# Kernel optimization log

Measured on AMD Instinct MI355X. Metric: run time of the kernel, lower is better.

Reference implementation:

```python
import jax, jax.numpy as jnp
import numpy as np

N = 100_000   # num nodes
E = 1_000_000 # num edges
F = 64        # feat_dim
H = 64        # hidden_dim
D = 64        # embed_dim


def _xavier(key, shape):
    limit = float(np.sqrt(6.0 / (shape[0] + shape[1])))
    return jax.random.uniform(key, shape, jnp.float32, -limit, limit)


def setup_inputs() -> dict:
    key = jax.random.key(0)
    ks = jax.random.split(key, 8)
    x = jax.random.normal(ks[0], (N, F), jnp.float32)
    edge_index = jax.random.randint(ks[1], (2, E), 0, N, dtype=jnp.int64)
    # GCNConv weights stored [in, out] (torch Linear transposed); biases zero-init
    return {
        "x": x,
        "edge_index": edge_index,
        "W1": _xavier(ks[2], (F, H)), "b1": jnp.zeros((H,), jnp.float32),
        "W2": _xavier(ks[3], (H, H)), "b2": jnp.zeros((H,), jnp.float32),
        "W3": _xavier(ks[4], (H, D)), "b3": jnp.zeros((D,), jnp.float32),
        "fw1": _xavier(ks[5], (D, H)), "fb1": jnp.zeros((H,), jnp.float32),
        "fw2": _xavier(ks[6], (H, D)), "fb2": jnp.zeros((D,), jnp.float32),
    }


def _gcn_conv(x, src, dst, dinv, W, b):
    # GCNConv: out = D^{-1/2} (A+I) D^{-1/2} (x W) + b
    h = x @ W                                   # [N, out]
    norm = dinv[src] * dinv[dst]                # [E]
    msg = h[src] * norm[:, None]                # gather + scale: [E, out]
    agg = jax.ops.segment_sum(msg, dst, num_segments=N)
    agg = agg + h * (dinv * dinv)[:, None]      # self-loop term
    return agg + b


def reference(x, edge_index, W1, b1, W2, b2, W3, b3, fw1, fb1, fw2, fb2):
    src, dst = edge_index[0], edge_index[1]
    # degree with self-loops (symmetric normalization)
    deg = jax.ops.segment_sum(jnp.ones((E,), x.dtype), dst, num_segments=N) + 1.0
    dinv = jax.lax.rsqrt(deg)
    # eval mode: dropout(p=0.5, training=False) is identity
    h = jax.nn.relu(_gcn_conv(x, src, dst, dinv, W1, b1))
    h = jax.nn.relu(_gcn_conv(h, src, dst, dinv, W2, b2))
    h = jax.nn.relu(_gcn_conv(h, src, dst, dinv, W3, b3))
    h = jax.nn.relu(h @ fw1 + fb1)
    return h @ fw2 + fb2                        # node embeddings [N, D]
```

## Files before the change

kernel.cpp:

```cpp
#include <hip/hip_runtime.h>
#include <cstdint>
#include <cstddef>


#define CDIV(a, b) (((a) + (b) - 1) / (b))

typedef __attribute__((ext_vector_type(8))) short bf16x8;
typedef __attribute__((ext_vector_type(4))) float f32x4;

static constexpr int BKT_SHIFT = 9;
static constexpr int BKT_NODES = 1 << BKT_SHIFT;
static constexpr int BKT_CAP = 7424;

__device__ __forceinline__ void split_bf(float a, short& hi, short& lo) {
  unsigned u = __float_as_uint(a);
  unsigned r = u + (0x7FFF + ((u >> 16) & 1));
  hi = (short)(r >> 16);
  float hirec = __uint_as_float(r & 0xFFFF0000u);
  float res = a - hirec;
  lo = (short)(__float_as_uint(res) >> 16);
}

__device__ __forceinline__ unsigned short f2bf_rne(float a) {
  unsigned u = __float_as_uint(a);
  u += 0x7FFF + ((u >> 16) & 1);
  return (unsigned short)(u >> 16);
}

__device__ __forceinline__ float4 bf4_to_f4(uint2 u) {
  float4 v;
  v.x = __uint_as_float(u.x << 16);
  v.y = __uint_as_float(u.x & 0xFFFF0000u);
  v.z = __uint_as_float(u.y << 16);
  v.w = __uint_as_float(u.y & 0xFFFF0000u);
  return v;
}

__device__ __forceinline__ void split8(float4 x, float4 y, bf16x8& h, bf16x8& l) {
  float av[8] = {x.x, x.y, x.z, x.w, y.x, y.y, y.z, y.w};
#pragma unroll
  for (int j = 0; j < 8; ++j) {
    short hi, lo;
    split_bf(av[j], hi, lo);
    h[j] = hi;
    l[j] = lo;
  }
}

__device__ __forceinline__ float4 nt_ld4(const float* p) {
  f32x4 v = __builtin_nontemporal_load(reinterpret_cast<const f32x4*>(p));
  float4 r;
  r.x = v[0]; r.y = v[1]; r.z = v[2]; r.w = v[3];
  return r;
}

__global__ __launch_bounds__(256)
void k_bucket(const int* __restrict__ ei, int* __restrict__ bcnt,
              int2* __restrict__ pairs, int E) {
  __shared__ int hist[256], rbase[256], roff[256];
  int t = threadIdx.x;
  int chunk = (E + gridDim.x - 1) / gridDim.x;
  int e0 = blockIdx.x * chunk;
  int e1 = min(e0 + chunk, E);
  hist[t] = 0;
  __syncthreads();
  for (int e = e0 + t; e < e1; e += 256) {
    int d = __builtin_nontemporal_load(&ei[E + e]);
    atomicAdd(&hist[d >> BKT_SHIFT], 1);
  }
  __syncthreads();
  roff[t] = 0;
  rbase[t] = hist[t] ? atomicAdd(&bcnt[t], hist[t]) : 0;
  __syncthreads();
  for (int e = e0 + t; e < e1; e += 256) {
    int d = __builtin_nontemporal_load(&ei[E + e]);
    int s = __builtin_nontemporal_load(&ei[e]);
    int b = d >> BKT_SHIFT;
    int r = atomicAdd(&roff[b], 1);
    int idx = rbase[b] + r;
    if (idx < BKT_CAP) pairs[(size_t)b * BKT_CAP + idx] = make_int2(s, d);
  }
}

__global__ __launch_bounds__(1024)
void k_build(const int2* __restrict__ pairs, const int* __restrict__ bcnt,
             int* __restrict__ row_ptr, float* __restrict__ dinv,
             int* __restrict__ srcs, int N, int E, int K) {
  __shared__ int cnt[BKT_NODES];
  __shared__ int deg[BKT_NODES];
  __shared__ int ebase_sh;
  int b = blockIdx.x;
  int t = threadIdx.x;
  int lo = b << BKT_SHIFT;
  int range = min(BKT_NODES, N - lo);
  int sz = min(bcnt[b], BKT_CAP);
  if (t == 0) {
    int s = 0;
    for (int i = 0; i < b; ++i) s += bcnt[i];
    ebase_sh = s;
  }
  if (t < BKT_NODES) cnt[t] = 0;
  __syncthreads();
  int ebase = ebase_sh;
  const int2* pb = pairs + (size_t)b * BKT_CAP;
  for (int i = t; i < sz; i += 1024) {
    atomicAdd(&cnt[pb[i].y - lo], 1);
  }
  __syncthreads();
  if (t < BKT_NODES) deg[t] = cnt[t];
  __syncthreads();
  int offset = 1;
  for (int d2 = BKT_NODES / 2; d2 > 0; d2 >>= 1) {
    if (t < d2) {
      int ai = offset * (2 * t + 1) - 1;
      int bi = offset * (2 * t + 2) - 1;
      cnt[bi] += cnt[ai];
    }
    offset <<= 1;
    __syncthreads();
  }
  if (t == 0) cnt[BKT_NODES - 1] = 0;
  __syncthreads();
  for (int d2 = 1; d2 < BKT_NODES; d2 <<= 1) {
    offset >>= 1;
    if (t < d2) {
      int ai = offset * (2 * t + 1) - 1;
      int bi = offset * (2 * t + 2) - 1;
      int tmp = cnt[ai];
      cnt[ai] = cnt[bi];
      cnt[bi] += tmp;
    }
    __syncthreads();
  }
  if (t < range) {
    row_ptr[lo + t] = ebase + cnt[t];
    dinv[lo + t] = rsqrtf((float)deg[t] + 1.0f);
  }
  if (b == K - 1 && t == 0) row_ptr[N] = E;
  __syncthreads();
  for (int i = t; i < sz; i += 1024) {
    int2 p = pb[i];
    int pos = ebase + atomicAdd(&cnt[p.y - lo], 1);
    srcs[pos] = p.x;
  }
}

__global__ void k_prep(const float* __restrict__ w0, const float* __restrict__ w1,
                       const float* __restrict__ w2, const float* __restrict__ w3,
                       const float* __restrict__ w4, bf16x8* __restrict__ packed,
                       int* __restrict__ bcnt) {
  if (blockIdx.x == 5) {
    if (threadIdx.x < 256) bcnt[threadIdx.x] = 0;
    return;
  }
  const float* W;
  switch (blockIdx.x) {
    case 0: W = w0; break;
    case 1: W = w1; break;
    case 2: W = w2; break;
    case 3: W = w3; break;
    default: W = w4; break;
  }
  int tid = threadIdx.x;
  int lane = tid & 63;
  int q = (tid >> 6) & 1;
  int t = tid >> 7;
  int col = lane & 15, quad = lane >> 4;
  bf16x8 hi8, lo8;
#pragma unroll
  for (int j = 0; j < 8; ++j) {
    int k = q * 32 + quad * 8 + j;
    short hi, lo;
    split_bf(W[k * 64 + t * 16 + col], hi, lo);
    hi8[j] = hi;
    lo8[j] = lo;
  }
  size_t base = (size_t)blockIdx.x * 1024 + ((t * 2 + q) * 2) * 64 + lane;
  packed[base] = hi8;
  packed[base + 64] = lo8;
}

__global__ __launch_bounds__(256, 4)
void k_mm(const float* __restrict__ in, const bf16x8* __restrict__ Wp,
          const float* __restrict__ dinv, unsigned short* __restrict__ out, int n) {
  if (blockIdx.x == 0 && threadIdx.x < 32) {
    ((unsigned int*)out)[(size_t)n * 32 + threadIdx.x] = 0u;
  }
  int lane = threadIdx.x & 63;
  int col = lane & 15, quad = lane >> 4;
  int tile = (blockIdx.x * blockDim.x + threadIdx.x) >> 6;
  int ntiles = (n + 15) >> 4;
  if (tile >= ntiles) return;

  bf16x8 wh[4][2], wl[4][2];
#pragma unroll
  for (int t = 0; t < 4; ++t)
#pragma unroll
    for (int q = 0; q < 2; ++q) {
      wh[t][q] = Wp[((t * 2 + q) * 2) * 64 + lane];
      wl[t][q] = Wp[((t * 2 + q) * 2 + 1) * 64 + lane];
    }

  int row0 = tile << 4;
  int ar = row0 + col;
  if (ar > n - 1) ar = n - 1;
  const float* arow = in + (size_t)ar * 64 + quad * 8;
  float4 a0 = nt_ld4(arow), a1 = nt_ld4(arow + 4);
  float4 a2 = nt_ld4(arow + 32), a3 = nt_ld4(arow + 36);

  bf16x8 ah[2], al[2];
  split8(a0, a1, ah[0], al[0]);
  split8(a2, a3, ah[1], al[1]);

  f32x4 acc[4];
#pragma unroll
  for (int t = 0; t < 4; ++t) acc[t] = (f32x4){0.f, 0.f, 0.f, 0.f};
#pragma unroll
  for (int t = 0; t < 4; ++t)
#pragma unroll
    for (int q = 0; q < 2; ++q) {
      acc[t] = __builtin_amdgcn_mfma_f32_16x16x32_bf16(ah[q], wh[t][q], acc[t], 0, 0, 0);
      acc[t] = __builtin_amdgcn_mfma_f32_16x16x32_bf16(ah[q], wl[t][q], acc[t], 0, 0, 0);
      acc[t] = __builtin_amdgcn_mfma_f32_16x16x32_bf16(al[q], wh[t][q], acc[t], 0, 0, 0);
    }
  float dv[4];
#pragma unroll
  for (int r = 0; r < 4; ++r) {
    int row = row0 + quad * 4 + r;
    dv[r] = (row < n) ? dinv[row] : 0.0f;
  }
#pragma unroll
  for (int t = 0; t < 4; ++t)
#pragma unroll
    for (int r = 0; r < 4; ++r) {
      int row = row0 + quad * 4 + r;
      if (row < n) out[(size_t)row * 64 + t * 16 + col] = f2bf_rne(acc[t][r] * dv[r]);
    }
}

template <bool HEAD>
__global__ __launch_bounds__(256, 6)
void k_agg_mm(const unsigned short* __restrict__ hws, const float* __restrict__ dinv,
              const int* __restrict__ row_ptr, const int* __restrict__ srcs,
              const float* __restrict__ bagg,
              const bf16x8* __restrict__ Wp1, const float* __restrict__ b1p,
              const bf16x8* __restrict__ Wp2, const float* __restrict__ b2p,
              void* __restrict__ out, int n) {
  constexpr int LDP = 68;
  __shared__ float a_sh[16 * LDP];
  int tid = threadIdx.x;
  int g = tid >> 4;
  int fg = tid & 15;
  int row0 = blockIdx.x << 4;
  const uint2* hw2 = (const uint2*)hws;

  if (!HEAD && blockIdx.x == 0 && tid < 32) {
    ((unsigned int*)out)[(size_t)n * 32 + tid] = 0u;
  }

  int node = row0 + g;
  bool valid = node < n;
  int nd = valid ? node : n;
  uint2 su = hw2[(size_t)nd * 16 + fg];
  float di = valid ? dinv[node] : 0.f;
  int p0 = 0, p1 = 0;
  if (valid) {
    p0 = row_ptr[node];
    p1 = row_ptr[node + 1];
  }
  float4 acc = make_float4(0.f, 0.f, 0.f, 0.f);
  if (p0 < p1) {
    int s[16];
#pragma unroll
    for (int j = 0; j < 16; ++j) {
      int ij = p0 + j;
      bool ok = ij < p1;
      int sv = __builtin_nontemporal_load(&srcs[ok ? ij : p1 - 1]);
      s[j] = ok ? sv : n;
    }
    uint2 u[16];
#pragma unroll
    for (int j = 0; j < 16; ++j) u[j] = hw2[(size_t)s[j] * 16 + fg];
#pragma unroll
    for (int j = 0; j < 16; ++j) {
      float4 v = bf4_to_f4(u[j]);
      acc.x += v.x;
      acc.y += v.y;
      acc.z += v.z;
      acc.w += v.w;
    }
    for (int p = p0 + 16; p < p1; p += 8) {
      int s2[8];
#pragma unroll
      for (int j = 0; j < 8; ++j) {
        int ij = p + j;
        bool ok = ij < p1;
        int sv = __builtin_nontemporal_load(&srcs[ok ? ij : p1 - 1]);
        s2[j] = ok ? sv : n;
      }
      uint2 u2[8];
#pragma unroll
      for (int j = 0; j < 8; ++j) u2[j] = hw2[(size_t)s2[j] * 16 + fg];
#pragma unroll
      for (int j = 0; j < 8; ++j) {
        float4 v = bf4_to_f4(u2[j]);
        acc.x += v.x;
        acc.y += v.y;
        acc.z += v.z;
        acc.w += v.w;
      }
    }
  }
  {
    float4 selfv = bf4_to_f4(su);
    float4 b4 = ((const float4*)bagg)[fg];
    float4 r = make_float4(0.f, 0.f, 0.f, 0.f);
    if (valid) {
      r.x = fmaxf(fmaf(di, acc.x + selfv.x, b4.x), 0.f);
      r.y = fmaxf(fmaf(di, acc.y + selfv.y, b4.y), 0.f);
      r.z = fmaxf(fmaf(di, acc.z + selfv.z, b4.z), 0.f);
      r.w = fmaxf(fmaf(di, acc.w + selfv.w, b4.w), 0.f);
    }
    *(float4*)&a_sh[g * LDP + (fg << 2)] = r;
  }
  __syncthreads();

  int lane = tid & 63;
  int wave = tid >> 6;
  int col = lane & 15, quad = lane >> 4;
  const float* arow = &a_sh[col * LDP + (quad << 3)];
  float4 a0 = *(const float4*)(arow);
  float4 a1 = *(const float4*)(arow + 4);
  float4 a2 = *(const float4*)(arow + 32);
  float4 a3 = *(const float4*)(arow + 36);
  bf16x8 ah[2], al[2];
  split8(a0, a1, ah[0], al[0]);
  split8(a2, a3, ah[1], al[1]);

  bf16x8 wh[2], wl[2];
#pragma unroll
  for (int q = 0; q < 2; ++q) {
    wh[q] = Wp1[((wave * 2 + q) * 2) * 64 + lane];
    wl[q] = Wp1[((wave * 2 + q) * 2 + 1) * 64 + lane];
  }
  f32x4 acc1 = (f32x4){0.f, 0.f, 0.f, 0.f};
#pragma unroll
  for (int q = 0; q < 2; ++q) {
    acc1 = __builtin_amdgcn_mfma_f32_16x16x32_bf16(ah[q], wh[q], acc1, 0, 0, 0);
    acc1 = __builtin_amdgcn_mfma_f32_16x16x32_bf16(ah[q], wl[q], acc1, 0, 0, 0);
    acc1 = __builtin_amdgcn_mfma_f32_16x16x32_bf16(al[q], wh[q], acc1, 0, 0, 0);
  }

  if constexpr (!HEAD) {
#pragma unroll
    for (int r = 0; r < 4; ++r) {
      int row = row0 + (quad << 2) + r;
      if (row < n) {
        ((unsigned short*)out)[(size_t)row * 64 + wave * 16 + col] =
            f2bf_rne(acc1[r] * dinv[row]);
      }
    }
  } else {
    float bv1 = b1p[wave * 16 + col];
    __syncthreads();
#pragma unroll
    for (int r = 0; r < 4; ++r) {
      a_sh[((quad << 2) + r) * LDP + wave * 16 + col] = fmaxf(acc1[r] + bv1, 0.f);
    }
    __syncthreads();
    const float* hrow = &a_sh[col * LDP + (quad << 3)];
    float4 h0 = *(const float4*)(hrow);
    float4 h1 = *(const float4*)(hrow + 4);
    float4 h2 = *(const float4*)(hrow + 32);
    float4 h3 = *(const float4*)(hrow + 36);
    bf16x8 ah2[2], al2[2];
    split8(h0, h1, ah2[0], al2[0]);
    split8(h2, h3, ah2[1], al2[1]);
    bf16x8 wh2[2], wl2[2];
#pragma unroll
    for (int q = 0; q < 2; ++q) {
      wh2[q] = Wp2[((wave * 2 + q) * 2) * 64 + lane];
      wl2[q] = Wp2[((wave * 2 + q) * 2 + 1) * 64 + lane];
    }
    f32x4 acc2 = (f32x4){0.f, 0.f, 0.f, 0.f};
#pragma unroll
    for (int q = 0; q < 2; ++q) {
      acc2 = __builtin_amdgcn_mfma_f32_16x16x32_bf16(ah2[q], wh2[q], acc2, 0, 0, 0);
      acc2 = __builtin_amdgcn_mfma_f32_16x16x32_bf16(ah2[q], wl2[q], acc2, 0, 0, 0);
      acc2 = __builtin_amdgcn_mfma_f32_16x16x32_bf16(al2[q], wh2[q], acc2, 0, 0, 0);
    }
    float bv2 = b2p[wave * 16 + col];
#pragma unroll
    for (int r = 0; r < 4; ++r) {
      int row = row0 + (quad << 2) + r;
      if (row < n) {
        ((float*)out)[(size_t)row * 64 + wave * 16 + col] = acc2[r] + bv2;
      }
    }
  }
}

extern "C" void kernel_launch(void* const* d_in, const int* in_sizes, int n_in,
                              void* d_out, int out_size, void* d_ws, size_t ws_size,
                              hipStream_t stream) {
  const float* x = (const float*)d_in[0];
  const int* ei = (const int*)d_in[1];
  const float* W1 = (const float*)d_in[2];
  const float* b1 = (const float*)d_in[3];
  const float* W2 = (const float*)d_in[4];
  const float* b2 = (const float*)d_in[5];
  const float* W3 = (const float*)d_in[6];
  const float* b3 = (const float*)d_in[7];
  const float* fw1 = (const float*)d_in[8];
  const float* fb1 = (const float*)d_in[9];
  const float* fw2 = (const float*)d_in[10];
  const float* fb2 = (const float*)d_in[11];
  float* out = (float*)d_out;

  const int N = in_sizes[0] / 64;
  const int E = in_sizes[1] / 2;
  const int K = CDIV(N, BKT_NODES);

  char* w = (char*)d_ws;
  auto take = [&](size_t bytes) -> char* {
    char* p = w;
    w += (bytes + 255) & ~(size_t)255;
    return p;
  };
  float* dinv = (float*)take((size_t)N * 4);
  int* row_ptr = (int*)take((size_t)(N + 1) * 4);
  int* bcnt = (int*)take((size_t)256 * 4);
  int* srcs = (int*)take((size_t)E * 4);
  bf16x8* wpack = (bf16x8*)take((size_t)5 * 1024 * 16);
  unsigned short* hwsA = (unsigned short*)take((size_t)(N + 1) * 64 * 2);
  unsigned short* hwsB = (unsigned short*)take((size_t)(N + 1) * 64 * 2);
  int2* pairs = (int2*)hwsA;

  const int B = 256;

  k_prep<<<6, 512, 0, stream>>>(W1, W2, W3, fw1, fw2, wpack, bcnt);
  k_bucket<<<512, B, 0, stream>>>(ei, bcnt, pairs, E);
  k_build<<<K, 1024, 0, stream>>>(pairs, bcnt, row_ptr, dinv, srcs, N, E, K);

  const int ntiles = CDIV(N, 16);
  const int MMG = CDIV(ntiles, 4);

  k_mm<<<MMG, B, 0, stream>>>(x, wpack + 0 * 1024, dinv, hwsA, N);
  k_agg_mm<false><<<ntiles, B, 0, stream>>>(hwsA, dinv, row_ptr, srcs, b1,
                                            wpack + 1 * 1024, nullptr, nullptr, nullptr,
                                            hwsB, N);
  k_agg_mm<false><<<ntiles, B, 0, stream>>>(hwsB, dinv, row_ptr, srcs, b2,
                                            wpack + 2 * 1024, nullptr, nullptr, nullptr,
                                            hwsA, N);
  k_agg_mm<true><<<ntiles, B, 0, stream>>>(hwsA, dinv, row_ptr, srcs, b3,
                                           wpack + 3 * 1024, fb1, wpack + 4 * 1024, fb2,
                                           out, N);
}
```

Before: 243.6 us.

## Store bf16 hidden features in per-wave column slabs for gather locality

Changes the intermediate bf16 feature buffer from row-major [N+1,64] to four column slabs of [N+1,16], and remaps aggregation threads so each wave gathers one 16-feature slab across 16 nodes. Each gathered neighbor row becomes a 32-byte segment within a smaller slab. The aim is for concurrently running waves to touch a narrower working set and so get better cache hit rates on the random gathers. In exchange each 64-byte row is split into four separate 32-byte accesses, which may raise transaction count, and workspace sizing must fit the new layout.

Result: slower. 333.2 us (+36.8%).

```diff
diff --git a/kernel.cpp b/kernel.cpp
--- a/kernel.cpp
+++ b/kernel.cpp
@@ -183,8 +183,10 @@
 __global__ __launch_bounds__(256, 4)
 void k_mm(const float* __restrict__ in, const bf16x8* __restrict__ Wp,
           const float* __restrict__ dinv, unsigned short* __restrict__ out, int n) {
-  if (blockIdx.x == 0 && threadIdx.x < 32) {
-    ((unsigned int*)out)[(size_t)n * 32 + threadIdx.x] = 0u;
+  size_t slabS = (size_t)(n + 1) * 16;
+  if (blockIdx.x == 0 && threadIdx.x < 64) {
+    int t = threadIdx.x >> 4, c = threadIdx.x & 15;
+    out[(size_t)t * slabS + (size_t)n * 16 + c] = 0;
   }
   int lane = threadIdx.x & 63;
   int col = lane & 15, quad = lane >> 4;
@@ -234,7 +236,9 @@
 #pragma unroll
     for (int r = 0; r < 4; ++r) {
       int row = row0 + quad * 4 + r;
-      if (row < n) out[(size_t)row * 64 + t * 16 + col] = f2bf_rne(acc[t][r] * dv[r]);
+      if (row < n) {
+        out[(size_t)t * slabS + (size_t)row * 16 + col] = f2bf_rne(acc[t][r] * dv[r]);
+      }
     }
 }
 
@@ -249,19 +253,23 @@
   constexpr int LDP = 68;
   __shared__ float a_sh[16 * LDP];
   int tid = threadIdx.x;
-  int g = tid >> 4;
-  int fg = tid & 15;
+  int w = tid >> 6;
+  int lane = tid & 63;
+  int g = lane >> 2;
+  int q = lane & 3;
   int row0 = blockIdx.x << 4;
-  const uint2* hw2 = (const uint2*)hws;
-
-  if (!HEAD && blockIdx.x == 0 && tid < 32) {
-    ((unsigned int*)out)[(size_t)n * 32 + tid] = 0u;
+  size_t slabS = (size_t)(n + 1) * 16;
+  const uint2* hw2 = (const uint2*)hws + (size_t)w * ((size_t)(n + 1) * 4);
+
+  if (!HEAD && blockIdx.x == 0 && tid < 64) {
+    int t = tid >> 4, c = tid & 15;
+    ((unsigned short*)out)[(size_t)t * slabS + (size_t)n * 16 + c] = 0;
   }
 
   int node = row0 + g;
   bool valid = node < n;
   int nd = valid ? node : n;
-  uint2 su = hw2[(size_t)nd * 16 + fg];
+  uint2 su = hw2[(size_t)nd * 4 + q];
   float di = valid ? dinv[node] : 0.f;
   int p0 = 0, p1 = 0;
   if (valid) {
@@ -280,7 +288,7 @@
     }
     uint2 u[16];
 #pragma unroll
-    for (int j = 0; j < 16; ++j) u[j] = hw2[(size_t)s[j] * 16 + fg];
+    for (int j = 0; j < 16; ++j) u[j] = hw2[(size_t)s[j] * 4 + q];
 #pragma unroll
     for (int j = 0; j < 16; ++j) {
       float4 v = bf4_to_f4(u[j]);
@@ -300,7 +308,7 @@
       }
       uint2 u2[8];
 #pragma unroll
-      for (int j = 0; j < 8; ++j) u2[j] = hw2[(size_t)s2[j] * 16 + fg];
+      for (int j = 0; j < 8; ++j) u2[j] = hw2[(size_t)s2[j] * 4 + q];
 #pragma unroll
       for (int j = 0; j < 8; ++j) {
         float4 v = bf4_to_f4(u2[j]);
@@ -313,7 +321,7 @@
   }
   {
     float4 selfv = bf4_to_f4(su);
-    float4 b4 = ((const float4*)bagg)[fg];
+    float4 b4 = ((const float4*)bagg)[w * 4 + q];
     float4 r = make_float4(0.f, 0.f, 0.f, 0.f);
     if (valid) {
       r.x = fmaxf(fmaf(di, acc.x + selfv.x, b4.x), 0.f);
@@ -321,12 +329,11 @@
       r.z = fmaxf(fmaf(di, acc.z + selfv.z, b4.z), 0.f);
       r.w = fmaxf(fmaf(di, acc.w + selfv.w, b4.w), 0.f);
     }
-    *(float4*)&a_sh[g * LDP + (fg << 2)] = r;
-  }
-  __syncthreads();
-
-  int lane = tid & 63;
-  int wave = tid >> 6;
+    *(float4*)&a_sh[g * LDP + w * 16 + (q << 2)] = r;
+  }
+  __syncthreads();
+
+  int wave = w;
   int col = lane & 15, quad = lane >> 4;
   const float* arow = &a_sh[col * LDP + (quad << 3)];
   float4 a0 = *(const float4*)(arow);
@@ -339,16 +346,16 @@
 
   bf16x8 wh[2], wl[2];
 #pragma unroll
-  for (int q = 0; q < 2; ++q) {
-    wh[q] = Wp1[((wave * 2 + q) * 2) * 64 + lane];
-    wl[q] = Wp1[((wave * 2 + q) * 2 + 1) * 64 + lane];
+  for (int q2 = 0; q2 < 2; ++q2) {
+    wh[q2] = Wp1[((wave * 2 + q2) * 2) * 64 + lane];
+    wl[q2] = Wp1[((wave * 2 + q2) * 2 + 1) * 64 + lane];
   }
   f32x4 acc1 = (f32x4){0.f, 0.f, 0.f, 0.f};
 #pragma unroll
-  for (int q = 0; q < 2; ++q) {
-    acc1 = __builtin_amdgcn_mfma_f32_16x16x32_bf16(ah[q], wh[q], acc1, 0, 0, 0);
-    acc1 = __builtin_amdgcn_mfma_f32_16x16x32_bf16(ah[q], wl[q], acc1, 0, 0, 0);
-    acc1 = __builtin_amdgcn_mfma_f32_16x16x32_bf16(al[q], wh[q], acc1, 0, 0, 0);
+  for (int q2 = 0; q2 < 2; ++q2) {
+    acc1 = __builtin_amdgcn_mfma_f32_16x16x32_bf16(ah[q2], wh[q2], acc1, 0, 0, 0);
+    acc1 = __builtin_amdgcn_mfma_f32_16x16x32_bf16(ah[q2], wl[q2], acc1, 0, 0, 0);
+    acc1 = __builtin_amdgcn_mfma_f32_16x16x32_bf16(al[q2], wh[q2], acc1, 0, 0, 0);
   }
 
   if constexpr (!HEAD) {
@@ -356,7 +363,7 @@
     for (int r = 0; r < 4; ++r) {
       int row = row0 + (quad << 2) + r;
       if (row < n) {
-        ((unsigned short*)out)[(size_t)row * 64 + wave * 16 + col] =
+        ((unsigned short*)out)[(size_t)wave * slabS + (size_t)row * 16 + col] =
             f2bf_rne(acc1[r] * dinv[row]);
       }
     }
@@ -378,16 +385,16 @@
     split8(h2, h3, ah2[1], al2[1]);
     bf16x8 wh2[2], wl2[2];
 #pragma unroll
-    for (int q = 0; q < 2; ++q) {
-      wh2[q] = Wp2[((wave * 2 + q) * 2) * 64 + lane];
-      wl2[q] = Wp2[((wave * 2 + q) * 2 + 1) * 64 + lane];
+    for (int q2 = 0; q2 < 2; ++q2) {
+      wh2[q2] = Wp2[((wave * 2 + q2) * 2) * 64 + lane];
+      wl2[q2] = Wp2[((wave * 2 + q2) * 2 + 1) * 64 + lane];
     }
     f32x4 acc2 = (f32x4){0.f, 0.f, 0.f, 0.f};
 #pragma unroll
-    for (int q = 0; q < 2; ++q) {
-      acc2 = __builtin_amdgcn_mfma_f32_16x16x32_bf16(ah2[q], wh2[q], acc2, 0, 0, 0);
-      acc2 = __builtin_amdgcn_mfma_f32_16x16x32_bf16(ah2[q], wl2[q], acc2, 0, 0, 0);
-      acc2 = __builtin_amdgcn_mfma_f32_16x16x32_bf16(al2[q], wh2[q], acc2, 0, 0, 0);
+    for (int q2 = 0; q2 < 2; ++q2) {
+      acc2 = __builtin_amdgcn_mfma_f32_16x16x32_bf16(ah2[q2], wh2[q2], acc2, 0, 0, 0);
+      acc2 = __builtin_amdgcn_mfma_f32_16x16x32_bf16(ah2[q2], wl2[q2], acc2, 0, 0, 0);
+      acc2 = __builtin_amdgcn_mfma_f32_16x16x32_bf16(al2[q2], wh2[q2], acc2, 0, 0, 0);
     }
     float bv2 = b2p[wave * 16 + col];
 #pragma unroll
```
